# Kernel tuning notes

Hardware: AMD Instinct MI355X
Metric: run time of the kernel (lower is better)

## Reference

```python
import jax, jax.numpy as jnp
import numpy as np


def setup_inputs() -> dict:
    key = jax.random.key(0)
    ks = jax.random.split(key, 6)
    C, C8, W, H, B = 512, 64, 64, 64, 4
    x = jax.random.normal(ks[0], (B, C, W, H), dtype=jnp.float32)
    Wf = jax.random.normal(ks[1], (C8, C), dtype=jnp.float32) * (1.0 / np.sqrt(C))
    Wg = jax.random.normal(ks[2], (C8, C), dtype=jnp.float32) * (1.0 / np.sqrt(C))
    Wh = jax.random.normal(ks[3], (C8, C), dtype=jnp.float32) * (1.0 / np.sqrt(C))
    Wv = jax.random.normal(ks[4], (C, C8), dtype=jnp.float32) * (1.0 / np.sqrt(C8))
    gamma = jax.random.normal(ks[5], (1,), dtype=jnp.float32)
    return {"x": x, "Wf": Wf, "Wg": Wg, "Wh": Wh, "Wv": Wv, "gamma": gamma}


def reference(x, Wf, Wg, Wh, Wv, gamma):
    b, c, w, h = x.shape
    n = w * h
    xf = x.reshape(b, c, n)                       # [b, c, n]
    # 1x1 convs == channel-mixing GEMMs
    f = jnp.einsum('oc,bcn->bon', Wf, xf)         # [b, c8, n]
    g = jnp.einsum('oc,bcn->bon', Wg, xf)         # [b, c8, n]
    hmap = jnp.einsum('oc,bcn->bon', Wh, xf)      # [b, c8, n]
    # attn_map[b, i, j] = sum_c f[b, c, i] * g[b, c, j]  (f permuted as in torch)
    attn = jnp.einsum('bci,bcj->bij', f, g)       # [b, n, n]
    # unconventional softmax over dim=1 (rows / the i axis)
    attn = jax.nn.softmax(attn, axis=1)
    sa = jnp.einsum('bcn,bnj->bcj', hmap, attn)   # [b, c8, n]
    sa = sa.reshape(b, -1, w, h)                  # [b, c8, w, h]
    sa = jnp.einsum('oc,bcwh->bowh', Wv, sa)      # [b, c, w, h]
    out = sa * gamma[0] + x
    return out, sa
```

## Files before the change

### kernel.cpp

```cpp
#include <hip/hip_runtime.h>
#include <cstddef>

#define BB 4
#define CC 512
#define NN 4096

using half8  = __attribute__((ext_vector_type(8))) _Float16;
using half4  = __attribute__((ext_vector_type(4))) _Float16;
using short8 = __attribute__((ext_vector_type(8))) short;
using us8    = __attribute__((ext_vector_type(8))) unsigned short;
using f32x4  = __attribute__((ext_vector_type(4))) float;

__device__ __forceinline__ unsigned short f2bf(float x) {
    unsigned int u = __float_as_uint(x);
    u += 0x7fffu + ((u >> 16) & 1u);
    return (unsigned short)(u >> 16);
}

__global__ __launch_bounds__(256) void prep_kernel(
    const float* __restrict__ Wf, const float* __restrict__ Wg,
    const float* __restrict__ Wh, const float* __restrict__ Wv,
    _Float16* __restrict__ Wc16, _Float16* __restrict__ Wv16)
{
    int idx = blockIdx.x * 256 + threadIdx.x;
    int stride = gridDim.x * 256;
    const int N1 = 192 * 512, N2 = 512 * 64;
    for (int i = idx; i < N1 + N2; i += stride) {
        if (i < N1) {
            int row = i >> 9, c = i & 511;
            const float* src = (row < 64) ? Wf : ((row < 128) ? Wg : Wh);
            Wc16[i] = (_Float16)src[(row & 63) * 512 + c];
        } else {
            int k = i - N1;
            Wv16[k] = (_Float16)Wv[k];
        }
    }
}

__global__ __launch_bounds__(256) void proj_kernel(
    const float* __restrict__ x, const _Float16* __restrict__ Wc16,
    _Float16* __restrict__ Kf, _Float16* __restrict__ Qf,
    unsigned short* __restrict__ Vt)
{
    const int t    = threadIdx.x;
    const int w    = t >> 6;
    const int lane = t & 63;
    const int lh   = lane & 15;
    const int qd   = lane >> 4;
    const int b    = blockIdx.x >> 8;
    const int i0   = (blockIdx.x & 255) << 4;

    f32x4 acc[3];
    #pragma unroll
    for (int ot = 0; ot < 3; ot++) { acc[ot][0]=0.f; acc[ot][1]=0.f; acc[ot][2]=0.f; acc[ot][3]=0.f; }

    const float* xb = x + (size_t)b*CC*NN + i0 + lh;
    const _Float16* wb = Wc16 + (size_t)(w*48 + lh)*512 + qd*8;

    for (int ck = 0; ck < 16; ck++) {
        half8 xf;
        const float* xp = xb + (size_t)(ck*32 + qd*8)*NN;
        #pragma unroll
        for (int jj = 0; jj < 8; jj++)
            xf[jj] = (_Float16)xp[(size_t)jj * NN];
        #pragma unroll
        for (int ot = 0; ot < 3; ot++) {
            half8 wf = *(const half8*)(wb + (size_t)(ot*16)*512 + ck*32);
            acc[ot] = __builtin_amdgcn_mfma_f32_16x16x32_f16(wf, xf, acc[ot], 0, 0, 0);
        }
    }

    #pragma unroll
    for (int ot = 0; ot < 3; ot++) {
        int g16 = w*3 + ot;
        int m   = g16 >> 2;
        int obase = (g16 & 3)*16 + qd*4;
        int ig = i0 + lh;
        #pragma unroll
        for (int r = 0; r < 4; r++) {
            float v = acc[ot][r];
            int ol = obase + r;
            if (m == 0)       Kf[((size_t)b*NN + ig)*64 + ol] = (_Float16)v;
            else if (m == 1)  Qf[((size_t)b*NN + ig)*64 + ol] = (_Float16)v;
            else              Vt[((size_t)b*64 + ol)*NN + ig] = f2bf(v);
        }
    }
}

__global__ __launch_bounds__(256) void attn_kernel(
    const _Float16* __restrict__ Kf, const _Float16* __restrict__ Qf,
    const unsigned short* __restrict__ Vt,
    _Float16* __restrict__ Po16, float* __restrict__ Pl)
{
    __shared__ __align__(16) unsigned short Kbuf[2][128*64];
    __shared__ __align__(16) unsigned short Vbuf[2][64*128];
    __shared__ __align__(16) unsigned short Psh[4][16*64];

    const int t    = threadIdx.x;
    const int wv   = t >> 6;
    const int lane = t & 63;
    const int lh   = lane & 15;
    const int qd   = lane >> 4;

    const int B   = blockIdx.x;
    const int xcd = B & 7;
    const int rr  = B >> 3;
    const int b   = xcd >> 1;
    const int jt  = (rr & 31)*2 + (xcd & 1);
    const int s   = rr >> 5;
    const int j0  = (jt << 6) + wv*16;

    const unsigned short* Kfu = (const unsigned short*)Kf;

    half8 qf0, qf1;
    {
        const size_t qb = ((size_t)b*NN + j0 + lh)*64 + qd*8;
        qf0 = *(const half8*)(Qf + qb);
        qf1 = *(const half8*)(Qf + qb + 32);
    }

    f32x4 o_acc[4];
    float l_r[4];
    #pragma unroll
    for (int dt = 0; dt < 4; dt++) { o_acc[dt][0]=0.f; o_acc[dt][1]=0.f; o_acc[dt][2]=0.f; o_acc[dt][3]=0.f; }
    #pragma unroll
    for (int r = 0; r < 4; r++) l_r[r] = 0.f;

    const int koff = s*1024;
    const int ki = t >> 3, kc = t & 7;
    const int vd = t >> 4, vc = t & 15;

#define LOADC(ck) do {                                                        \
    size_t kg = ((size_t)b*NN + koff + (ck)*128)*64;                          \
    size_t vg = (size_t)b*64*NN + koff + (ck)*128;                            \
    _Pragma("unroll")                                                         \
    for (int r_ = 0; r_ < 4; r_++) {                                          \
        kst[r_] = *(const us8*)(Kfu + kg + (size_t)(r_*32 + ki)*64 + kc*8);   \
        vst[r_] = *(const us8*)(Vt  + vg + (size_t)(r_*16 + vd)*NN + vc*8);   \
    } } while (0)

#define STOREC(p_) do {                                                       \
    _Pragma("unroll")                                                         \
    for (int r_ = 0; r_ < 4; r_++) {                                          \
        int i_ = r_*32 + ki;                                                  \
        int d_ = r_*16 + vd;                                                  \
        *(us8*)(&Kbuf[p_][i_*64  + ((kc ^ (i_ & 7))*8)])  = kst[r_];          \
        *(us8*)(&Vbuf[p_][d_*128 + ((vc ^ (d_ & 15))*8)]) = vst[r_];          \
    } } while (0)

    us8 kst[4], vst[4];
    LOADC(0);
    STOREC(0);
    __syncthreads();

    for (int ck = 0; ck < 8; ck++) {
        const int p = ck & 1;
        if (ck < 7) LOADC(ck + 1);

        #pragma unroll
        for (int half = 0; half < 2; half++) {
            const unsigned short* Kb = &Kbuf[p][half*64*64];
            const unsigned short* Vb = &Vbuf[p][0];

            f32x4 sc[4];
            #pragma unroll
            for (int it = 0; it < 4; it++) {
                sc[it][0]=0.f; sc[it][1]=0.f; sc[it][2]=0.f; sc[it][3]=0.f;
                const unsigned short* kr = Kb + (it*16 + lh)*64;
                half8 k0 = *(const half8*)(kr + ((qd     ^ (lh & 7))*8));
                half8 k1 = *(const half8*)(kr + (((4+qd) ^ (lh & 7))*8));
                sc[it] = __builtin_amdgcn_mfma_f32_16x16x32_f16(qf0, k0, sc[it], 0,0,0);
                sc[it] = __builtin_amdgcn_mfma_f32_16x16x32_f16(qf1, k1, sc[it], 0,0,0);
            }

            #pragma unroll
            for (int it = 0; it < 4; it++)
                #pragma unroll
                for (int r = 0; r < 4; r++) {
                    float p_ = __expf(sc[it][r]);
                    l_r[r] += p_;
                    int i_ = it*16 + lh;
                    int j_ = qd*4 + r;
                    Psh[wv][j_*64 + (((i_>>3) ^ (j_ & 7))*8) + (i_ & 7)] = f2bf(p_);
                }
            asm volatile("s_waitcnt lgkmcnt(0)" ::: "memory");

            short8 pf0 = *(const short8*)&Psh[wv][lh*64 + ((qd     ^ (lh & 7))*8)];
            short8 pf1 = *(const short8*)&Psh[wv][lh*64 + (((4+qd) ^ (lh & 7))*8)];

            #pragma unroll
            for (int dt = 0; dt < 4; dt++) {
                const unsigned short* vr = Vb + (dt*16 + lh)*128;
                short8 v0 = *(const short8*)(vr + (((half*8 + qd    ) ^ lh)*8));
                short8 v1 = *(const short8*)(vr + (((half*8 + 4 + qd) ^ lh)*8));
                o_acc[dt] = __builtin_amdgcn_mfma_f32_16x16x32_bf16(pf0, v0, o_acc[dt], 0,0,0);
                o_acc[dt] = __builtin_amdgcn_mfma_f32_16x16x32_bf16(pf1, v1, o_acc[dt], 0,0,0);
            }
        }

        if (ck < 7) STOREC(p ^ 1);
        __syncthreads();
    }
#undef LOADC
#undef STOREC

    float inv[4];
    #pragma unroll
    for (int r = 0; r < 4; r++) {
        float l = l_r[r];
        #pragma unroll
        for (int off = 1; off < 16; off <<= 1)
            l += __shfl_xor(l, off);
        l_r[r] = l;
        inv[r] = 1.0f / l;
    }
    const size_t pbase = ((size_t)(s*4 + b)*NN + j0);
    #pragma unroll
    for (int dt = 0; dt < 4; dt++)
        #pragma unroll
        for (int r = 0; r < 4; r++)
            Po16[(pbase + qd*4 + r)*64 + dt*16 + lh] = (_Float16)(o_acc[dt][r] * inv[r]);
    if (lh == 0) {
        #pragma unroll
        for (int r = 0; r < 4; r++)
            Pl[pbase + qd*4 + r] = l_r[r];
    }
}

__global__ __launch_bounds__(256) void combine_kernel(
    const _Float16* __restrict__ Po16, const float* __restrict__ Pl,
    _Float16* __restrict__ sa16)
{
    int tid = blockIdx.x * 256 + threadIdx.x;
    int d4  = (tid & 15) * 4;
    int j   = (tid >> 4) & 4095;
    int b   = tid >> 16;
    float o0 = 0.f, o1 = 0.f, o2 = 0.f, o3 = 0.f, lsum = 0.f;
    #pragma unroll
    for (int s = 0; s < 4; s++) {
        size_t base = ((size_t)(s*4 + b)*NN + j);
        half4 v = *(const half4*)(Po16 + base*64 + d4);
        float l = Pl[base];
        o0 += l * (float)v[0]; o1 += l * (float)v[1];
        o2 += l * (float)v[2]; o3 += l * (float)v[3];
        lsum += l;
    }
    float inv = 1.0f / lsum;
    half4 r;
    r[0] = (_Float16)(o0 * inv); r[1] = (_Float16)(o1 * inv);
    r[2] = (_Float16)(o2 * inv); r[3] = (_Float16)(o3 * inv);
    *(half4*)(sa16 + ((size_t)b*NN + j)*64 + d4) = r;
}

__global__ __launch_bounds__(256) void outproj_kernel(
    const _Float16* __restrict__ sa16, const _Float16* __restrict__ Wv16,
    const float* __restrict__ x, const float* __restrict__ gamma,
    float* __restrict__ out1, float* __restrict__ out2)
{
    const int t    = threadIdx.x;
    const int w    = t >> 6;
    const int lane = t & 63;
    const int lh   = lane & 15;
    const int qd   = lane >> 4;
    const int b    = blockIdx.x >> 7;
    const int j0   = (blockIdx.x & 127) << 5;
    const float g  = gamma[0];

    half8 sb[2][2];
    #pragma unroll
    for (int jt2 = 0; jt2 < 2; jt2++) {
        const size_t sbase = ((size_t)b*NN + j0 + jt2*16 + lh)*64 + qd*8;
        sb[jt2][0] = *(const half8*)(sa16 + sbase);
        sb[jt2][1] = *(const half8*)(sa16 + sbase + 32);
    }

    #pragma unroll 2
    for (int ot8 = 0; ot8 < 8; ot8++) {
        const int ot = w*8 + ot8;
        const size_t wbase = (size_t)(ot*16 + lh)*64 + qd*8;
        half8 a0 = *(const half8*)(Wv16 + wbase);
        half8 a1 = *(const half8*)(Wv16 + wbase + 32);
        #pragma unroll
        for (int jt2 = 0; jt2 < 2; jt2++) {
            f32x4 acc; acc[0]=0.f; acc[1]=0.f; acc[2]=0.f; acc[3]=0.f;
            acc = __builtin_amdgcn_mfma_f32_16x16x32_f16(a0, sb[jt2][0], acc, 0, 0, 0);
            acc = __builtin_amdgcn_mfma_f32_16x16x32_f16(a1, sb[jt2][1], acc, 0, 0, 0);
            const int jg = j0 + jt2*16 + lh;
            #pragma unroll
            for (int r = 0; r < 4; r++) {
                const int o = ot*16 + qd*4 + r;
                size_t idx = ((size_t)b*CC + o)*NN + jg;
                float v = acc[r];
                out2[idx] = v;
                out1[idx] = fmaf(g, v, x[idx]);
            }
        }
    }
}

extern "C" void kernel_launch(void* const* d_in, const int* in_sizes, int n_in,
                              void* d_out, int out_size, void* d_ws, size_t ws_size,
                              hipStream_t stream) {
    const float* x     = (const float*)d_in[0];
    const float* Wf    = (const float*)d_in[1];
    const float* Wg    = (const float*)d_in[2];
    const float* Wh    = (const float*)d_in[3];
    const float* Wv    = (const float*)d_in[4];
    const float* gamma = (const float*)d_in[5];

    float* out1 = (float*)d_out;
    float* out2 = out1 + (size_t)BB*CC*NN;

    const size_t BND = (size_t)BB*NN*64;
    char* wp = (char*)d_ws;
    _Float16*       Kf   = (_Float16*)wp;        wp += BND*2;
    _Float16*       Qf   = (_Float16*)wp;        wp += BND*2;
    unsigned short* Vt   = (unsigned short*)wp;  wp += BND*2;
    _Float16*       Po16 = (_Float16*)wp;        wp += BND*4*2;
    float*          Pl   = (float*)wp;           wp += (size_t)4*BB*NN*4;
    _Float16*       Wc16 = (_Float16*)wp;        wp += (size_t)192*512*2;
    _Float16*       Wv16 = (_Float16*)wp;
    _Float16*       sa16 = Kf;

    prep_kernel<<<dim3(64), dim3(256), 0, stream>>>(Wf, Wg, Wh, Wv, Wc16, Wv16);
    proj_kernel<<<dim3(BB*256), dim3(256), 0, stream>>>(x, Wc16, Kf, Qf, Vt);
    attn_kernel<<<dim3(BB*256), dim3(256), 0, stream>>>(Kf, Qf, Vt, Po16, Pl);
    combine_kernel<<<dim3(1024), dim3(256), 0, stream>>>(Po16, Pl, sa16);
    outproj_kernel<<<dim3(512), dim3(256), 0, stream>>>(sa16, Wv16, x, gamma, out1, out2);
}
```

Measured before the change: 183.7 us.

## Stage x through LDS in proj, fold log2e into Wg, fuse combine into outproj

```diff
diff --git a/kernel.cpp b/kernel.cpp
--- a/kernel.cpp
+++ b/kernel.cpp
@@ -6,7 +6,7 @@
 #define NN 4096
 
 using half8  = __attribute__((ext_vector_type(8))) _Float16;
-using half4  = __attribute__((ext_vector_type(4))) _Float16;
+using fp16x2 = __attribute__((ext_vector_type(2))) __fp16;
 using short8 = __attribute__((ext_vector_type(8))) short;
 using us8    = __attribute__((ext_vector_type(8))) unsigned short;
 using f32x4  = __attribute__((ext_vector_type(4))) float;
@@ -29,7 +29,8 @@
         if (i < N1) {
             int row = i >> 9, c = i & 511;
             const float* src = (row < 64) ? Wf : ((row < 128) ? Wg : Wh);
-            Wc16[i] = (_Float16)src[(row & 63) * 512 + c];
+            float sc = (row >= 64 && row < 128) ? 1.4426950408889634f : 1.0f;
+            Wc16[i] = (_Float16)(sc * src[(row & 63) * 512 + c]);
         } else {
             int k = i - N1;
             Wv16[k] = (_Float16)Wv[k];
@@ -42,6 +43,7 @@
     _Float16* __restrict__ Kf, _Float16* __restrict__ Qf,
     unsigned short* __restrict__ Vt)
 {
+    __shared__ float xsT[2][16][68];
     const int t    = threadIdx.x;
     const int w    = t >> 6;
     const int lane = t & 63;
@@ -54,20 +56,44 @@
     #pragma unroll
     for (int ot = 0; ot < 3; ot++) { acc[ot][0]=0.f; acc[ot][1]=0.f; acc[ot][2]=0.f; acc[ot][3]=0.f; }
 
-    const float* xb = x + (size_t)b*CC*NN + i0 + lh;
-    const _Float16* wb = Wc16 + (size_t)(w*48 + lh)*512 + qd*8;
-
-    for (int ck = 0; ck < 16; ck++) {
-        half8 xf;
-        const float* xp = xb + (size_t)(ck*32 + qd*8)*NN;
-        #pragma unroll
-        for (int jj = 0; jj < 8; jj++)
-            xf[jj] = (_Float16)xp[(size_t)jj * NN];
-        #pragma unroll
-        for (int ot = 0; ot < 3; ot++) {
-            half8 wf = *(const half8*)(wb + (size_t)(ot*16)*512 + ck*32);
-            acc[ot] = __builtin_amdgcn_mfma_f32_16x16x32_f16(wf, xf, acc[ot], 0, 0, 0);
-        }
+    const int ti = t & 3;
+    const int tc = t >> 2;
+    const float* xbase = x + (size_t)b*CC*NN + i0 + ti*4;
+
+    float4 st = *(const float4*)(xbase + (size_t)tc*NN);
+    xsT[0][ti*4+0][tc] = st.x; xsT[0][ti*4+1][tc] = st.y;
+    xsT[0][ti*4+2][tc] = st.z; xsT[0][ti*4+3][tc] = st.w;
+    __syncthreads();
+
+    for (int ck = 0; ck < 8; ck++) {
+        const int p = ck & 1;
+        if (ck < 7) st = *(const float4*)(xbase + (size_t)((ck+1)*64 + tc)*NN);
+
+        #pragma unroll
+        for (int ks = 0; ks < 2; ks++) {
+            half8 wf[3];
+            #pragma unroll
+            for (int ot = 0; ot < 3; ot++)
+                wf[ot] = *(const half8*)(Wc16 + (size_t)(w*48 + ot*16 + lh)*512 + ck*64 + ks*32 + qd*8);
+            const float* xr = &xsT[p][lh][ks*32 + qd*8];
+            f32x4 xa = *(const f32x4*)xr;
+            f32x4 xb = *(const f32x4*)(xr + 4);
+            union { fp16x2 h2[4]; half8 h8; } u;
+            u.h2[0] = __builtin_amdgcn_cvt_pkrtz(xa[0], xa[1]);
+            u.h2[1] = __builtin_amdgcn_cvt_pkrtz(xa[2], xa[3]);
+            u.h2[2] = __builtin_amdgcn_cvt_pkrtz(xb[0], xb[1]);
+            u.h2[3] = __builtin_amdgcn_cvt_pkrtz(xb[2], xb[3]);
+            #pragma unroll
+            for (int ot = 0; ot < 3; ot++)
+                acc[ot] = __builtin_amdgcn_mfma_f32_16x16x32_f16(wf[ot], u.h8, acc[ot], 0, 0, 0);
+        }
+
+        if (ck < 7) {
+            const int q = p ^ 1;
+            xsT[q][ti*4+0][tc] = st.x; xsT[q][ti*4+1][tc] = st.y;
+            xsT[q][ti*4+2][tc] = st.z; xsT[q][ti*4+3][tc] = st.w;
+        }
+        __syncthreads();
     }
 
     #pragma unroll
@@ -92,8 +118,8 @@
     const unsigned short* __restrict__ Vt,
     _Float16* __restrict__ Po16, float* __restrict__ Pl)
 {
-    __shared__ __align__(16) unsigned short Kbuf[2][128*64];
-    __shared__ __align__(16) unsigned short Vbuf[2][64*128];
+    __shared__ __align__(16) unsigned short Kbuf[128*64];
+    __shared__ __align__(16) unsigned short Vbuf[64*128];
     __shared__ __align__(16) unsigned short Psh[4][16*64];
 
     const int t    = threadIdx.x;
@@ -139,28 +165,27 @@
         vst[r_] = *(const us8*)(Vt  + vg + (size_t)(r_*16 + vd)*NN + vc*8);   \
     } } while (0)
 
-#define STOREC(p_) do {                                                       \
+#define STOREC() do {                                                         \
     _Pragma("unroll")                                                         \
     for (int r_ = 0; r_ < 4; r_++) {                                          \
         int i_ = r_*32 + ki;                                                  \
         int d_ = r_*16 + vd;                                                  \
-        *(us8*)(&Kbuf[p_][i_*64  + ((kc ^ (i_ & 7))*8)])  = kst[r_];          \
-        *(us8*)(&Vbuf[p_][d_*128 + ((vc ^ (d_ & 15))*8)]) = vst[r_];          \
+        *(us8*)(&Kbuf[i_*64  + ((kc ^ (i_ & 7))*8)])  = kst[r_];              \
+        *(us8*)(&Vbuf[d_*128 + ((vc ^ (d_ & 15))*8)]) = vst[r_];              \
     } } while (0)
 
     us8 kst[4], vst[4];
     LOADC(0);
-    STOREC(0);
+    STOREC();
     __syncthreads();
 
     for (int ck = 0; ck < 8; ck++) {
-        const int p = ck & 1;
         if (ck < 7) LOADC(ck + 1);
 
         #pragma unroll
         for (int half = 0; half < 2; half++) {
-            const unsigned short* Kb = &Kbuf[p][half*64*64];
-            const unsigned short* Vb = &Vbuf[p][0];
+            const unsigned short* Kb = &Kbuf[half*64*64];
+            const unsigned short* Vb = &Vbuf[0];
 
             f32x4 sc[4];
             #pragma unroll
@@ -177,7 +202,7 @@
             for (int it = 0; it < 4; it++)
                 #pragma unroll
                 for (int r = 0; r < 4; r++) {
-                    float p_ = __expf(sc[it][r]);
+                    float p_ = exp2f(sc[it][r]);
                     l_r[r] += p_;
                     int i_ = it*16 + lh;
                     int j_ = qd*4 + r;
@@ -198,7 +223,8 @@
             }
         }
 
-        if (ck < 7) STOREC(p ^ 1);
+        __syncthreads();
+        if (ck < 7) STOREC();
         __syncthreads();
     }
 #undef LOADC
@@ -227,33 +253,9 @@
     }
 }
 
-__global__ __launch_bounds__(256) void combine_kernel(
+__global__ __launch_bounds__(256) void outproj_kernel(
     const _Float16* __restrict__ Po16, const float* __restrict__ Pl,
-    _Float16* __restrict__ sa16)
-{
-    int tid = blockIdx.x * 256 + threadIdx.x;
-    int d4  = (tid & 15) * 4;
-    int j   = (tid >> 4) & 4095;
-    int b   = tid >> 16;
-    float o0 = 0.f, o1 = 0.f, o2 = 0.f, o3 = 0.f, lsum = 0.f;
-    #pragma unroll
-    for (int s = 0; s < 4; s++) {
-        size_t base = ((size_t)(s*4 + b)*NN + j);
-        half4 v = *(const half4*)(Po16 + base*64 + d4);
-        float l = Pl[base];
-        o0 += l * (float)v[0]; o1 += l * (float)v[1];
-        o2 += l * (float)v[2]; o3 += l * (float)v[3];
-        lsum += l;
-    }
-    float inv = 1.0f / lsum;
-    half4 r;
-    r[0] = (_Float16)(o0 * inv); r[1] = (_Float16)(o1 * inv);
-    r[2] = (_Float16)(o2 * inv); r[3] = (_Float16)(o3 * inv);
-    *(half4*)(sa16 + ((size_t)b*NN + j)*64 + d4) = r;
-}
-
-__global__ __launch_bounds__(256) void outproj_kernel(
-    const _Float16* __restrict__ sa16, const _Float16* __restrict__ Wv16,
+    const _Float16* __restrict__ Wv16,
     const float* __restrict__ x, const float* __restrict__ gamma,
     float* __restrict__ out1, float* __restrict__ out2)
 {
@@ -269,9 +271,33 @@
     half8 sb[2][2];
     #pragma unroll
     for (int jt2 = 0; jt2 < 2; jt2++) {
-        const size_t sbase = ((size_t)b*NN + j0 + jt2*16 + lh)*64 + qd*8;
-        sb[jt2][0] = *(const half8*)(sa16 + sbase);
-        sb[jt2][1] = *(const half8*)(sa16 + sbase + 32);
+        const int j = j0 + jt2*16 + lh;
+        float os[16];
+        #pragma unroll
+        for (int k = 0; k < 16; k++) os[k] = 0.f;
+        float lsum = 0.f;
+        #pragma unroll
+        for (int s = 0; s < 4; s++) {
+            size_t base = ((size_t)(s*4 + b)*NN + j);
+            half8 v0 = *(const half8*)(Po16 + base*64 + qd*8);
+            half8 v1 = *(const half8*)(Po16 + base*64 + qd*8 + 32);
+            float l = Pl[base];
+            #pragma unroll
+            for (int k = 0; k < 8; k++) {
+                os[k]   = fmaf(l, (float)v0[k], os[k]);
+                os[8+k] = fmaf(l, (float)v1[k], os[8+k]);
+            }
+            lsum += l;
+        }
+        float inv = 1.0f / lsum;
+        union { fp16x2 h2[4]; half8 h8; } u0, u1;
+        #pragma unroll
+        for (int k = 0; k < 4; k++) {
+            u0.h2[k] = __builtin_amdgcn_cvt_pkrtz(os[2*k]*inv,   os[2*k+1]*inv);
+            u1.h2[k] = __builtin_amdgcn_cvt_pkrtz(os[8+2*k]*inv, os[8+2*k+1]*inv);
+        }
+        sb[jt2][0] = u0.h8;
+        sb[jt2][1] = u1.h8;
     }
 
     #pragma unroll 2
@@ -320,11 +346,9 @@
     float*          Pl   = (float*)wp;           wp += (size_t)4*BB*NN*4;
     _Float16*       Wc16 = (_Float16*)wp;        wp += (size_t)192*512*2;
     _Float16*       Wv16 = (_Float16*)wp;
-    _Float16*       sa16 = Kf;
 
     prep_kernel<<<dim3(64), dim3(256), 0, stream>>>(Wf, Wg, Wh, Wv, Wc16, Wv16);
     proj_kernel<<<dim3(BB*256), dim3(256), 0, stream>>>(x, Wc16, Kf, Qf, Vt);
     attn_kernel<<<dim3(BB*256), dim3(256), 0, stream>>>(Kf, Qf, Vt, Po16, Pl);
-    combine_kernel<<<dim3(1024), dim3(256), 0, stream>>>(Po16, Pl, sa16);
-    outproj_kernel<<<dim3(512), dim3(256), 0, stream>>>(sa16, Wv16, x, gamma, out1, out2);
-}
+    outproj_kernel<<<dim3(512), dim3(256), 0, stream>>>(Po16, Pl, Wv16, x, gamma, out1, out2);
+}
```

Measured after the change: 187.8 us. 1.02x slower.
